# Optimization experiments

Hardware: AMD Instinct MI355X
Metric: run time of the kernel (lower is better)

Reference implementation:

```python
import jax, jax.numpy as jnp
import numpy as np
import math

D_MODEL = 1024
N_HEADS = 16
HEAD_DIM = D_MODEL // N_HEADS


def setup_inputs() -> dict:
    key = jax.random.key(0)
    k1, k2, k3 = jax.random.split(key, 3)
    B, T = 2, 2048
    x = jax.random.normal(k1, (B, T, D_MODEL), dtype=jnp.float32)
    W_qkv = jax.random.normal(k2, (D_MODEL, 3 * D_MODEL), dtype=jnp.float32) * (1.0 / math.sqrt(D_MODEL))
    W_out = jax.random.normal(k3, (D_MODEL, D_MODEL), dtype=jnp.float32) * (1.0 / math.sqrt(D_MODEL))
    return {"x": x, "W_qkv": W_qkv, "W_out": W_out}


def reference(x, W_qkv, W_out):
    B, T, C = x.shape
    qkv = x @ W_qkv  # [B, T, 3C]
    q, k, v = jnp.split(qkv, 3, axis=-1)

    def heads(t):  # [B,T,C] -> [B,H,T,Dh]
        return t.reshape(B, T, N_HEADS, HEAD_DIM).transpose(0, 2, 1, 3)

    q, k, v = heads(q), heads(k), heads(v)
    scale = 1.0 / math.sqrt(HEAD_DIM)
    scores = jnp.einsum('bhtd,bhsd->bhts', q, k) * scale  # [B,H,T,T]
    causal = jnp.tril(jnp.ones((T, T), dtype=bool))
    scores = jnp.where(causal[None, None, :, :], scores, -jnp.inf)
    attn = jax.nn.softmax(scores, axis=-1)
    out = jnp.einsum('bhts,bhsd->bhtd', attn, v)  # [B,H,T,Dh]
    out = out.transpose(0, 2, 1, 3).reshape(B, T, C)
    return out @ W_out
```

## Files before the change

kernel.cpp:

```cpp
#include <hip/hip_runtime.h>
#include <hip/hip_bf16.h>

typedef __bf16 bf16;
typedef bf16 bf16x4 __attribute__((ext_vector_type(4)));
typedef bf16 bf16x8 __attribute__((ext_vector_type(8)));
typedef float f32x4 __attribute__((ext_vector_type(4)));
typedef float f32x16 __attribute__((ext_vector_type(16)));
typedef unsigned int u32x4 __attribute__((ext_vector_type(4)));

#define GLOAD16(g, l) __builtin_amdgcn_global_load_lds( \
    (const __attribute__((address_space(1))) void*)(g),  \
    (__attribute__((address_space(3))) void*)(l), 16, 0, 0)

#define EXP2F(x) __builtin_amdgcn_exp2f(x)
#define MFMA16(a, b, c) __builtin_amdgcn_mfma_f32_16x16x32_bf16(a, b, c, 0, 0, 0)
#define MFMA32(a, b, c) __builtin_amdgcn_mfma_f32_32x32x16_bf16(a, b, c, 0, 0, 0)

__global__ __launch_bounds__(256) void prep(const float* __restrict__ x,
                                            const float* __restrict__ Wqkv,
                                            const float* __restrict__ Wout,
                                            bf16* __restrict__ xb,
                                            bf16* __restrict__ wqkvT,
                                            bf16* __restrict__ woutT) {
  int id = blockIdx.x, tid = threadIdx.x;
  if (id < 2048) {
    int i = id * 256 + tid;
    const float4* p = (const float4*)x + (size_t)i * 2;
    float4 a = p[0], b = p[1];
    bf16x8 o;
    o[0] = (bf16)a.x; o[1] = (bf16)a.y; o[2] = (bf16)a.z; o[3] = (bf16)a.w;
    o[4] = (bf16)b.x; o[5] = (bf16)b.y; o[6] = (bf16)b.z; o[7] = (bf16)b.w;
    ((bf16x8*)xb)[i] = o;
  } else {
    __shared__ float tile[32][33];
    const float* src; bf16* dst; int N, j;
    if (id < 5120) { src = Wqkv; dst = wqkvT; N = 3072; j = id - 2048; }
    else           { src = Wout; dst = woutT; N = 1024; j = id - 5120; }
    int ntile = N / 32;
    int n0 = (j % ntile) * 32, k0 = (j / ntile) * 32;
    int tx = tid & 31, ty = tid >> 5;
#pragma unroll
    for (int i = 0; i < 4; i++)
      tile[ty + 8 * i][tx] = src[(size_t)(k0 + ty + 8 * i) * N + n0 + tx];
    __syncthreads();
#pragma unroll
    for (int i = 0; i < 4; i++)
      dst[(size_t)(n0 + ty + 8 * i) * 1024 + k0 + tx] = (bf16)tile[tx][ty + 8 * i];
  }
}

__device__ __forceinline__ void gemm_mainloop64(const bf16* __restrict__ A,
                                                const bf16* __restrict__ Bt,
                                                int K, int m0, int n0,
                                                f32x4 acc[4][4],
                                                bf16* As, bf16* Bs) {
  int tid = threadIdx.x;
  int lane = tid & 63;
  int wave = tid >> 6;
  int wr = wave >> 1, wc = wave & 1;
  int c16 = lane & 15, g = lane >> 4;
  f32x4 z = {0.f, 0.f, 0.f, 0.f};
#pragma unroll
  for (int m = 0; m < 4; m++)
#pragma unroll
    for (int n = 0; n < 4; n++) acc[m][n] = z;
  for (int k0 = 0; k0 < K; k0 += 64) {
#pragma unroll
    for (int i = 0; i < 4; i++) {
      int cc = tid + i * 256;
      int r = cc >> 3, ch = cc & 7;
      int sc = ch ^ (r & 7);
      GLOAD16(A + (size_t)(m0 + r) * K + k0 + sc * 8, As + cc * 8);
    }
#pragma unroll
    for (int i = 0; i < 4; i++) {
      int cc = tid + i * 256;
      int r = cc >> 3, ch = cc & 7;
      int sc = ch ^ (r & 7);
      GLOAD16(Bt + (size_t)(n0 + r) * K + k0 + sc * 8, Bs + cc * 8);
    }
    __syncthreads();
#pragma unroll
    for (int h = 0; h < 2; h++) {
      bf16x8 af[4], bfr[4];
#pragma unroll
      for (int m = 0; m < 4; m++) {
        int ar = wr * 64 + m * 16 + c16;
        af[m] = *(const bf16x8*)((const char*)As + ar * 128 + (((h * 4 + g) ^ (ar & 7)) << 4));
      }
#pragma unroll
      for (int n = 0; n < 4; n++) {
        int br = wc * 64 + n * 16 + c16;
        bfr[n] = *(const bf16x8*)((const char*)Bs + br * 128 + (((h * 4 + g) ^ (br & 7)) << 4));
      }
      __builtin_amdgcn_s_setprio(1);
#pragma unroll
      for (int m = 0; m < 4; m++)
#pragma unroll
        for (int n = 0; n < 4; n++)
          acc[m][n] = MFMA16(af[m], bfr[n], acc[m][n]);
      __builtin_amdgcn_s_setprio(0);
    }
    __syncthreads();
  }
}

__global__ __launch_bounds__(256) void gemm_qkv(const bf16* __restrict__ A,
                                                const bf16* __restrict__ Bt,
                                                bf16* __restrict__ q,
                                                bf16* __restrict__ kk,
                                                bf16* __restrict__ vt) {
  __shared__ bf16 As[128 * 64];
  __shared__ bf16 Bs[128 * 64];
  int id = blockIdx.x;
  int xc = id & 7, k = id >> 3;
  int bn = xc * 3 + (k % 3), bm = k / 3;
  int m0 = bm * 128, n0 = bn * 128;
  f32x4 acc[4][4];
  gemm_mainloop64(A, Bt, 1024, m0, n0, acc, As, Bs);
  int lane = threadIdx.x & 63;
  int wave = threadIdx.x >> 6;
  int wr = wave >> 1, wc = wave & 1;
  int c16 = lane & 15, g = lane >> 4;
  int which = n0 >> 10;
  const float QSCALE = 0.125f * 1.4426950408889634f;
  if (which == 2) {
#pragma unroll
    for (int m = 0; m < 4; m++)
#pragma unroll
      for (int n = 0; n < 4; n++) {
        int gm0 = m0 + wr * 64 + m * 16 + g * 4;
        int gn = n0 + wc * 64 + n * 16 + c16;
        int rem = gn & 1023, h = rem >> 6, d = rem & 63;
        int b = gm0 >> 11, t0 = gm0 & 2047;
        size_t bh = (size_t)(b * 16 + h);
        bf16x4 pv;
        pv[0] = (bf16)acc[m][n][0]; pv[1] = (bf16)acc[m][n][1];
        pv[2] = (bf16)acc[m][n][2]; pv[3] = (bf16)acc[m][n][3];
        *(bf16x4*)(vt + (bh * 64 + d) * 2048 + t0) = pv;
      }
  } else {
#pragma unroll
    for (int m = 0; m < 4; m++)
#pragma unroll
      for (int n = 0; n < 4; n++)
#pragma unroll
        for (int j = 0; j < 4; j++) {
          int gm = m0 + wr * 64 + m * 16 + g * 4 + j;
          int gn = n0 + wc * 64 + n * 16 + c16;
          int rem = gn & 1023, h = rem >> 6, d = rem & 63;
          int b = gm >> 11, t = gm & 2047;
          float v = acc[m][n][j];
          size_t bh = (size_t)(b * 16 + h);
          if (which == 0) q[(bh * 2048 + t) * 64 + d]  = (bf16)(v * QSCALE);
          else            kk[(bh * 2048 + t) * 64 + d] = (bf16)v;
        }
  }
}

__global__ __launch_bounds__(256) void gemm_out(const bf16* __restrict__ A,
                                                const bf16* __restrict__ Bt,
                                                float* __restrict__ C) {
  __shared__ bf16 As[64 * 64];
  __shared__ bf16 Bs[128 * 64];
  int tid = threadIdx.x;
  int lane = tid & 63;
  int wave = tid >> 6;
  int wr = wave >> 1, wc = wave & 1;
  int c16 = lane & 15, g = lane >> 4;
  int id = blockIdx.x;
  int bn = id & 7, bm = id >> 3;
  int m0 = bm * 64, n0 = bn * 128;
  const int K = 1024;
  f32x4 acc[2][4];
  {
    f32x4 z = {0.f, 0.f, 0.f, 0.f};
#pragma unroll
    for (int m = 0; m < 2; m++)
#pragma unroll
      for (int n = 0; n < 4; n++) acc[m][n] = z;
  }
  for (int k0 = 0; k0 < K; k0 += 64) {
#pragma unroll
    for (int i = 0; i < 2; i++) {
      int cc = tid + i * 256;
      int r = cc >> 3, ch = cc & 7;
      int sc = ch ^ (r & 7);
      GLOAD16(A + (size_t)(m0 + r) * K + k0 + sc * 8, As + cc * 8);
    }
#pragma unroll
    for (int i = 0; i < 4; i++) {
      int cc = tid + i * 256;
      int r = cc >> 3, ch = cc & 7;
      int sc = ch ^ (r & 7);
      GLOAD16(Bt + (size_t)(n0 + r) * K + k0 + sc * 8, Bs + cc * 8);
    }
    __syncthreads();
#pragma unroll
    for (int h = 0; h < 2; h++) {
      bf16x8 af[2], bfr[4];
#pragma unroll
      for (int m = 0; m < 2; m++) {
        int ar = wr * 32 + m * 16 + c16;
        af[m] = *(const bf16x8*)((const char*)As + ar * 128 + (((h * 4 + g) ^ (ar & 7)) << 4));
      }
#pragma unroll
      for (int n = 0; n < 4; n++) {
        int br = wc * 64 + n * 16 + c16;
        bfr[n] = *(const bf16x8*)((const char*)Bs + br * 128 + (((h * 4 + g) ^ (br & 7)) << 4));
      }
      __builtin_amdgcn_s_setprio(1);
#pragma unroll
      for (int m = 0; m < 2; m++)
#pragma unroll
        for (int n = 0; n < 4; n++)
          acc[m][n] = MFMA16(af[m], bfr[n], acc[m][n]);
      __builtin_amdgcn_s_setprio(0);
    }
    __syncthreads();
  }
#pragma unroll
  for (int m = 0; m < 2; m++)
#pragma unroll
    for (int n = 0; n < 4; n++)
#pragma unroll
      for (int j = 0; j < 4; j++) {
        int gm = m0 + wr * 32 + m * 16 + g * 4 + j;
        int gn = n0 + wc * 64 + n * 16 + c16;
        C[(size_t)gm * 1024 + gn] = acc[m][n][j];
      }
}

__global__ __launch_bounds__(256) void attn(const bf16* __restrict__ q,
                                            const bf16* __restrict__ kk,
                                            const bf16* __restrict__ vt,
                                            bf16* __restrict__ out) {
  __shared__ bf16 Ks[4][64 * 64];
  __shared__ bf16 Vs[4][64 * 64];
  int tid = threadIdx.x, lane = tid & 63, w = tid >> 6;
  int ql = lane & 31, hi = lane >> 5;

  int id = blockIdx.x;
  int c = id & 7;
  int k = id >> 3;
  int s = k >> 5;
  int j5 = k & 31;
  int bxi = j5 & 15, b2 = j5 >> 4;
  int bx = s ? (15 - bxi) : bxi;
  int bh = 4 * c + 2 * b2 + s;
  int q0 = bx * 128;

  const bf16* qb = q  + (size_t)bh * 2048 * 64;
  const bf16* kb = kk + (size_t)bh * 2048 * 64;
  const bf16* vb = vt + (size_t)bh * 64 * 2048;
  int nt = 2 * bx + 2;
  int ns = nt >> 1;

  int qlo = q0 + w * 32;
  int qg = qlo + ql;

  bf16x8 qf[4];
#pragma unroll
  for (int j = 0; j < 4; j++)
    qf[j] = *(const bf16x8*)(qb + (size_t)qg * 64 + j * 16 + hi * 8);

#pragma unroll
  for (int i = 0; i < 2; i++) {
    int cc = tid + i * 256;
    int r = cc >> 3;
    int sw = ((cc & 7) ^ (r & 7)) * 8;
    GLOAD16(kb + (size_t)r * 64 + sw, Ks[0] + cc * 8);
    GLOAD16(vb + (size_t)r * 2048 + sw, Vs[0] + cc * 8);
    GLOAD16(kb + (size_t)(64 + r) * 64 + sw, Ks[1] + cc * 8);
    GLOAD16(vb + (size_t)r * 2048 + 64 + sw, Vs[1] + cc * 8);
  }
  __syncthreads();

  f32x16 o[2];
#pragma unroll
  for (int i = 0; i < 16; i++) { o[0][i] = 0.f; o[1][i] = 0.f; }
  float lsum = 0.f;

  for (int st = 0; st < ns; ++st) {
    if (st + 1 < ns) {
      int sn = st * 128 + 128;
      int nb = (2 * st + 2) & 3;
#pragma unroll
      for (int i = 0; i < 2; i++) {
        int cc = tid + i * 256;
        int r = cc >> 3;
        int sw = ((cc & 7) ^ (r & 7)) * 8;
        GLOAD16(kb + (size_t)(sn + r) * 64 + sw, Ks[nb] + cc * 8);
        GLOAD16(vb + (size_t)r * 2048 + sn + sw, Vs[nb] + cc * 8);
        GLOAD16(kb + (size_t)(sn + 64 + r) * 64 + sw, Ks[nb + 1] + cc * 8);
        GLOAD16(vb + (size_t)r * 2048 + sn + 64 + sw, Vs[nb + 1] + cc * 8);
      }
    }
#pragma unroll
    for (int half = 0; half < 2; ++half) {
      int t = 2 * st + half;
      int s0 = t * 64;
      if (s0 > qlo + 31) continue;
      const char* Kb = (const char*)Ks[t & 3];
      const char* Vb = (const char*)Vs[t & 3];
      f32x16 S[2];
#pragma unroll
      for (int i = 0; i < 16; i++) { S[0][i] = 0.f; S[1][i] = 0.f; }
      __builtin_amdgcn_s_setprio(1);
#pragma unroll
      for (int j = 0; j < 4; j++) {
        int row0 = ql, row1 = 32 + ql;
        bf16x8 kf0 = *(const bf16x8*)(Kb + row0 * 128 + (((2 * j + hi) ^ (row0 & 7)) << 4));
        bf16x8 kf1 = *(const bf16x8*)(Kb + row1 * 128 + (((2 * j + hi) ^ (row1 & 7)) << 4));
        S[0] = MFMA32(kf0, qf[j], S[0]);
        S[1] = MFMA32(kf1, qf[j], S[1]);
      }
      __builtin_amdgcn_s_setprio(0);
      if (s0 + 63 > qlo) {
#pragma unroll
        for (int sb = 0; sb < 2; sb++)
#pragma unroll
          for (int r = 0; r < 16; r++) {
            int sg = s0 + sb * 32 + (r & 3) + 8 * (r >> 2) + 4 * hi;
            if (sg > qg) S[sb][r] = -__builtin_inff();
          }
      }
#pragma unroll
      for (int sb = 0; sb < 2; sb++)
#pragma unroll
        for (int r = 0; r < 16; r++) {
          float pv2 = EXP2F(S[sb][r]);
          S[sb][r] = pv2;
          lsum += pv2;
        }
      __builtin_amdgcn_s_setprio(1);
#pragma unroll
      for (int j = 0; j < 4; j++) {
        int sb = j >> 1, rb = (j & 1) * 8;
        unsigned pa, pb, pc, pd;
        asm("v_cvt_pk_bf16_f32 %0, %1, %2" : "=v"(pa) : "v"(S[sb][rb + 0]), "v"(S[sb][rb + 1]));
        asm("v_cvt_pk_bf16_f32 %0, %1, %2" : "=v"(pb) : "v"(S[sb][rb + 2]), "v"(S[sb][rb + 3]));
        asm("v_cvt_pk_bf16_f32 %0, %1, %2" : "=v"(pc) : "v"(S[sb][rb + 4]), "v"(S[sb][rb + 5]));
        asm("v_cvt_pk_bf16_f32 %0, %1, %2" : "=v"(pd) : "v"(S[sb][rb + 6]), "v"(S[sb][rb + 7]));
        asm("v_permlane32_swap_b32 %0, %1" : "+v"(pa), "+v"(pc));
        asm("v_permlane32_swap_b32 %0, %1" : "+v"(pb), "+v"(pd));
        union { u32x4 u; bf16x8 h; } pu;
        pu.u[0] = pa; pu.u[1] = pb; pu.u[2] = pc; pu.u[3] = pd;
        int row0 = ql, row1 = 32 + ql;
        bf16x8 vf0 = *(const bf16x8*)(Vb + row0 * 128 + (((2 * j + hi) ^ (row0 & 7)) << 4));
        bf16x8 vf1 = *(const bf16x8*)(Vb + row1 * 128 + (((2 * j + hi) ^ (row1 & 7)) << 4));
        o[0] = MFMA32(vf0, pu.h, o[0]);
        o[1] = MFMA32(vf1, pu.h, o[1]);
      }
      __builtin_amdgcn_s_setprio(0);
    }
    if (st + 1 < ns) {
      asm volatile("s_waitcnt vmcnt(0)" ::: "memory");
      __builtin_amdgcn_s_barrier();
      __builtin_amdgcn_sched_barrier(0);
    }
  }
  lsum += __shfl_xor(lsum, 32);
  float inv = 1.f / lsum;
  int b = bh >> 4, h = bh & 15;
  size_t rowbase = ((size_t)(b * 2048 + qg)) * 1024 + h * 64;
#pragma unroll
  for (int db = 0; db < 2; db++)
#pragma unroll
    for (int qd = 0; qd < 4; qd++) {
      bf16x4 pv;
#pragma unroll
      for (int i = 0; i < 4; i++) pv[i] = (bf16)(o[db][4 * qd + i] * inv);
      *(bf16x4*)(out + rowbase + db * 32 + 8 * qd + 4 * hi) = pv;
    }
}

extern "C" void kernel_launch(void* const* d_in, const int* in_sizes, int n_in,
                              void* d_out, int out_size, void* d_ws, size_t ws_size,
                              hipStream_t stream) {
  const float* x    = (const float*)d_in[0];
  const float* Wqkv = (const float*)d_in[1];
  const float* Wout = (const float*)d_in[2];
  float* outp = (float*)d_out;
  char* ws = (char*)d_ws;
  const size_t MB = 1024 * 1024;
  bf16* xb    = (bf16*)(ws);
  bf16* wqkvT = (bf16*)(ws + 8 * MB);
  bf16* woutT = (bf16*)(ws + 14 * MB);
  bf16* qb    = (bf16*)(ws + 16 * MB);
  bf16* kb    = (bf16*)(ws + 24 * MB);
  bf16* vtb   = (bf16*)(ws + 32 * MB);

  hipLaunchKernelGGL(prep, dim3(6144), dim3(256), 0, stream,
                     x, Wqkv, Wout, xb, wqkvT, woutT);
  hipLaunchKernelGGL(gemm_qkv, dim3(768), dim3(256), 0, stream,
                     xb, wqkvT, qb, kb, vtb);
  hipLaunchKernelGGL(attn, dim3(512), dim3(256), 0, stream,
                     qb, kb, vtb, xb);
  hipLaunchKernelGGL(gemm_out, dim3(512), dim3(256), 0, stream,
                     xb, woutT, outp);
}
```

Baseline: 101.4 us.

## Split attention KV tiles across two wave groups and merge partial outputs in LDS

Doubles the attention block to 512 threads. The two groups of four waves each process alternating 64-key halves of every 128-key stage for the same query rows, instead of one wave handling both halves in sequence. At the end, group 1 writes its partial O accumulators and row sums to shared memory and group 0 adds them before normalising and storing. This trades an extra barrier, an LDS exchange and more registers per block for more parallelism in the per-block key loop. It relies on the softmax using a fixed offset rather than a running max, so the partial sums can simply be added.

```diff
diff --git a/kernel.cpp b/kernel.cpp
--- a/kernel.cpp
+++ b/kernel.cpp
@@ -231,13 +231,15 @@
       }
 }
 
-__global__ __launch_bounds__(256) void attn(const bf16* __restrict__ q,
-                                            const bf16* __restrict__ kk,
-                                            const bf16* __restrict__ vt,
-                                            bf16* __restrict__ out) {
-  __shared__ bf16 Ks[4][64 * 64];
-  __shared__ bf16 Vs[4][64 * 64];
+__global__ __launch_bounds__(512, 4) void attn(const bf16* __restrict__ q,
+                                               const bf16* __restrict__ kk,
+                                               const bf16* __restrict__ vt,
+                                               bf16* __restrict__ out) {
+  __shared__ __align__(16) char smem[65536];
+  bf16* Ks = (bf16*)smem;
+  bf16* Vs = (bf16*)(smem + 32768);
   int tid = threadIdx.x, lane = tid & 63, w = tid >> 6;
+  int qw = w & 3, par = w >> 2;
   int ql = lane & 31, hi = lane >> 5;
 
   int id = blockIdx.x;
@@ -256,7 +258,7 @@
   int nt = 2 * bx + 2;
   int ns = nt >> 1;
 
-  int qlo = q0 + w * 32;
+  int qlo = q0 + qw * 32;
   int qg = qlo + ql;
 
   bf16x8 qf[4];
@@ -264,15 +266,14 @@
   for (int j = 0; j < 4; j++)
     qf[j] = *(const bf16x8*)(qb + (size_t)qg * 64 + j * 16 + hi * 8);
 
-#pragma unroll
-  for (int i = 0; i < 2; i++) {
-    int cc = tid + i * 256;
+  {
+    int cc = tid;
     int r = cc >> 3;
     int sw = ((cc & 7) ^ (r & 7)) * 8;
-    GLOAD16(kb + (size_t)r * 64 + sw, Ks[0] + cc * 8);
-    GLOAD16(vb + (size_t)r * 2048 + sw, Vs[0] + cc * 8);
-    GLOAD16(kb + (size_t)(64 + r) * 64 + sw, Ks[1] + cc * 8);
-    GLOAD16(vb + (size_t)r * 2048 + 64 + sw, Vs[1] + cc * 8);
+    GLOAD16(kb + (size_t)r * 64 + sw, Ks + cc * 8);
+    GLOAD16(vb + (size_t)r * 2048 + sw, Vs + cc * 8);
+    GLOAD16(kb + (size_t)(64 + r) * 64 + sw, Ks + 4096 + cc * 8);
+    GLOAD16(vb + (size_t)r * 2048 + 64 + sw, Vs + 4096 + cc * 8);
   }
   __syncthreads();
 
@@ -285,24 +286,19 @@
     if (st + 1 < ns) {
       int sn = st * 128 + 128;
       int nb = (2 * st + 2) & 3;
-#pragma unroll
-      for (int i = 0; i < 2; i++) {
-        int cc = tid + i * 256;
-        int r = cc >> 3;
-        int sw = ((cc & 7) ^ (r & 7)) * 8;
-        GLOAD16(kb + (size_t)(sn + r) * 64 + sw, Ks[nb] + cc * 8);
-        GLOAD16(vb + (size_t)r * 2048 + sn + sw, Vs[nb] + cc * 8);
-        GLOAD16(kb + (size_t)(sn + 64 + r) * 64 + sw, Ks[nb + 1] + cc * 8);
-        GLOAD16(vb + (size_t)r * 2048 + sn + 64 + sw, Vs[nb + 1] + cc * 8);
-      }
-    }
-#pragma unroll
-    for (int half = 0; half < 2; ++half) {
-      int t = 2 * st + half;
-      int s0 = t * 64;
-      if (s0 > qlo + 31) continue;
-      const char* Kb = (const char*)Ks[t & 3];
-      const char* Vb = (const char*)Vs[t & 3];
+      int cc = tid;
+      int r = cc >> 3;
+      int sw = ((cc & 7) ^ (r & 7)) * 8;
+      GLOAD16(kb + (size_t)(sn + r) * 64 + sw, Ks + nb * 4096 + cc * 8);
+      GLOAD16(vb + (size_t)r * 2048 + sn + sw, Vs + nb * 4096 + cc * 8);
+      GLOAD16(kb + (size_t)(sn + 64 + r) * 64 + sw, Ks + (nb + 1) * 4096 + cc * 8);
+      GLOAD16(vb + (size_t)r * 2048 + sn + 64 + sw, Vs + (nb + 1) * 4096 + cc * 8);
+    }
+    int t = 2 * st + par;
+    int s0 = t * 64;
+    if (s0 <= qlo + 31) {
+      const char* Kb = (const char*)(Ks + (t & 3) * 4096);
+      const char* Vb = (const char*)(Vs + (t & 3) * 4096);
       f32x16 S[2];
 #pragma unroll
       for (int i = 0; i < 16; i++) { S[0][i] = 0.f; S[1][i] = 0.f; }
@@ -361,18 +357,37 @@
     }
   }
   lsum += __shfl_xor(lsum, 32);
-  float inv = 1.f / lsum;
-  int b = bh >> 4, h = bh & 15;
-  size_t rowbase = ((size_t)(b * 2048 + qg)) * 1024 + h * 64;
-#pragma unroll
-  for (int db = 0; db < 2; db++)
-#pragma unroll
-    for (int qd = 0; qd < 4; qd++) {
-      bf16x4 pv;
-#pragma unroll
-      for (int i = 0; i < 4; i++) pv[i] = (bf16)(o[db][4 * qd + i] * inv);
-      *(bf16x4*)(out + rowbase + db * 32 + 8 * qd + 4 * hi) = pv;
-    }
+  __syncthreads();
+  float* xch = (float*)smem;
+  if (par == 1) {
+    float* dst = xch + (qw * 64 + lane) * 33;
+#pragma unroll
+    for (int db = 0; db < 2; db++)
+#pragma unroll
+      for (int i = 0; i < 16; i++) dst[db * 16 + i] = o[db][i];
+    dst[32] = lsum;
+  }
+  __syncthreads();
+  if (par == 0) {
+    const float* src = xch + (qw * 64 + lane) * 33;
+#pragma unroll
+    for (int db = 0; db < 2; db++)
+#pragma unroll
+      for (int i = 0; i < 16; i++) o[db][i] += src[db * 16 + i];
+    lsum += src[32];
+    float inv = 1.f / lsum;
+    int b = bh >> 4, h = bh & 15;
+    size_t rowbase = ((size_t)(b * 2048 + qg)) * 1024 + h * 64;
+#pragma unroll
+    for (int db = 0; db < 2; db++)
+#pragma unroll
+      for (int qd = 0; qd < 4; qd++) {
+        bf16x4 pv;
+#pragma unroll
+        for (int i = 0; i < 4; i++) pv[i] = (bf16)(o[db][4 * qd + i] * inv);
+        *(bf16x4*)(out + rowbase + db * 32 + 8 * qd + 4 * hi) = pv;
+      }
+  }
 }
 
 extern "C" void kernel_launch(void* const* d_in, const int* in_sizes, int n_in,
@@ -395,7 +410,7 @@
                      x, Wqkv, Wout, xb, wqkvT, woutT);
   hipLaunchKernelGGL(gemm_qkv, dim3(768), dim3(256), 0, stream,
                      xb, wqkvT, qb, kb, vtb);
-  hipLaunchKernelGGL(attn, dim3(512), dim3(256), 0, stream,
+  hipLaunchKernelGGL(attn, dim3(512), dim3(512), 0, stream,
                      qb, kb, vtb, xb);
   hipLaunchKernelGGL(gemm_out, dim3(512), dim3(256), 0, stream,
                      xb, woutT, outp);
```

Measured after the change: 89.77 us (median of 2 runs). 1.13x faster.
